# Kernel tuning notes

Hardware: AMD Instinct MI355X
Metric: run time of the kernel (lower is better)

## Reference

```python
import jax, jax.numpy as jnp
import numpy as np

B, T, C, H = 4, 2048, 1024, 16
D = C // H  # head_dim = 64


def setup_inputs() -> dict:
    key = jax.random.key(0)
    k1, k2, k3, k4 = jax.random.split(key, 4)
    x = jax.random.normal(k1, (B, T, C), dtype=jnp.float32)
    # realistic padding: each sequence has length in [T//2, T]
    lengths = jax.random.randint(k4, (B,), T // 2, T + 1)
    padding_mask = jnp.arange(T)[None, :] < lengths[:, None]  # True = keep
    # weights stored [in, out] (equivalent to torch Linear weight transposed)
    w_qkv = jax.random.normal(k2, (C, 3 * C), dtype=jnp.float32) * (C ** -0.5)
    w_out = jax.random.normal(k3, (C, C), dtype=jnp.float32) * (C ** -0.5)
    b_out = jnp.zeros((C,), dtype=jnp.float32)
    return {"x": x, "padding_mask": padding_mask, "w_qkv": w_qkv, "w_out": w_out, "b_out": b_out}


def reference(x, padding_mask, w_qkv, w_out, b_out):
    scale = D ** -0.5
    qkv = x @ w_qkv  # [B,T,3C]
    q, k, v = jnp.split(qkv, 3, axis=-1)

    def split_heads(t):
        return t.reshape(B, T, H, D).transpose(0, 2, 1, 3)  # [B,H,T,D]

    q, k, v = split_heads(q), split_heads(k), split_heads(v)
    attn = jnp.einsum("bhqd,bhkd->bhqk", q, k) * scale  # [B,H,T,T]
    mask = padding_mask[:, None, None, :]  # [B,1,1,T]
    attn = jnp.where(mask, attn, jnp.finfo(attn.dtype).min)
    attn = jax.nn.softmax(attn, axis=-1)
    # dropout is identity in eval mode
    out = jnp.einsum("bhqk,bhkd->bhqd", attn, v)  # [B,H,T,D]
    out = out.transpose(0, 2, 1, 3).reshape(B, T, C)
    return out @ w_out + b_out
```

## Files before the change

### kernel.cpp

```cpp
#include <hip/hip_runtime.h>
#include <hip/hip_bf16.h>

#define Bb 4
#define Tt 2048
#define Cc 1024
#define Hh 16

typedef unsigned short u16;
typedef __attribute__((ext_vector_type(8))) __bf16 bf16x8;
typedef __attribute__((ext_vector_type(4))) float  f32x4;

__device__ __forceinline__ u16 f2bf(float f) {
    union { float f; unsigned u; } v; v.f = f;
    unsigned r = v.u + 0x7fff + ((v.u >> 16) & 1);
    return (u16)(r >> 16);
}

__device__ __forceinline__ u16 f2bf_hw(float f) {
    __bf16 h = (__bf16)f;
    return *(u16*)&h;
}

__device__ __forceinline__ float fexp2(float x) {
#if __has_builtin(__builtin_amdgcn_exp2f)
    return __builtin_amdgcn_exp2f(x);
#else
    return __expf(x * 0.6931471805599453f);
#endif
}

__device__ __forceinline__ void gld_lds16(const void* g, void* l) {
    __builtin_amdgcn_global_load_lds(
        (__attribute__((address_space(1))) void*)(g),
        (__attribute__((address_space(3))) void*)(l),
        16, 0, 0);
}

__device__ __forceinline__ f32x4 mfma16(bf16x8 a, bf16x8 b, f32x4 c) {
    return __builtin_amdgcn_mfma_f32_16x16x32_bf16(a, b, c, 0, 0, 0);
}

__global__ void cast_f32_bf16(const float* __restrict__ in, u16* __restrict__ out, int n4) {
    int i = blockIdx.x * 256 + threadIdx.x;
    if (i < n4) {
        float4 v = ((const float4*)in)[i];
        uint2 o;
        o.x = (unsigned)f2bf_hw(v.x) | ((unsigned)f2bf_hw(v.y) << 16);
        o.y = (unsigned)f2bf_hw(v.z) | ((unsigned)f2bf_hw(v.w) << 16);
        ((uint2*)out)[i] = o;
    }
}

__global__ void castT_f32_bf16(const float* __restrict__ in, u16* __restrict__ out,
                               int K, int N) {
    __shared__ float Ls[64][65];
    const int n0 = blockIdx.x * 64, k0 = blockIdx.y * 64;
    const int t = threadIdx.x;
    #pragma unroll
    for (int s = 0; s < 4; ++s) {
        int idx = t + 256 * s;
        int r   = idx >> 4;
        int c4  = (idx & 15) * 4;
        float4 v = *(const float4*)&in[(size_t)(k0 + r) * N + n0 + c4];
        Ls[r][c4 + 0] = v.x; Ls[r][c4 + 1] = v.y;
        Ls[r][c4 + 2] = v.z; Ls[r][c4 + 3] = v.w;
    }
    __syncthreads();
    #pragma unroll
    for (int s = 0; s < 2; ++s) {
        int idx = t + 256 * s;
        int n   = idx >> 3;
        int kc  = (idx & 7) * 8;
        alignas(16) u16 tmp[8];
        #pragma unroll
        for (int i = 0; i < 8; ++i) tmp[i] = f2bf_hw(Ls[kc + i][n]);
        *(uint4*)&out[(size_t)(n0 + n) * K + k0 + kc] = *(const uint4*)tmp;
    }
}

__global__ void repack_vT(const u16* __restrict__ qkv, u16* __restrict__ vT) {
    const int t = threadIdx.x, w = t >> 6, lane = t & 63;
    const int tile = blockIdx.x, bh = blockIdx.y, b = bh >> 4, h = bh & 15;
    #pragma unroll
    for (int u = 0; u < 2; ++u) {
        int tc = tile * 64 + (2 * w + u) * 8;
        alignas(16) u16 tmp[8];
        #pragma unroll
        for (int i = 0; i < 8; ++i)
            tmp[i] = qkv[(size_t)(b * Tt + tc + i) * (3 * Cc) + 2 * Cc + h * 64 + lane];
        *(uint4*)&vT[((size_t)(bh * 64) + lane) * Tt + tc] = *(const uint4*)tmp;
    }
}

__global__ __launch_bounds__(256, 3) void gemm_bt_bf16(
    const u16* __restrict__ A, const u16* __restrict__ Bt,
    const float* __restrict__ bias,
    u16* __restrict__ outB, float* __restrict__ outF,
    int M, int N, int K)
{
    __shared__ u16 As[128 * 32];
    __shared__ u16 Bs[128 * 32];
    const int t = threadIdx.x;
    const int w = t >> 6, lane = t & 63;
    const int quad = lane >> 4, l16 = lane & 15;
    const int wr = w >> 1, wc = w & 1;
    const int m0 = blockIdx.y * 128, n0 = blockIdx.x * 128;

    int aoff[4], boff[4];
    #pragma unroll
    for (int i = 0; i < 4; ++i) {
        int rA = 64 * wr + 16 * i + l16;
        aoff[i] = rA * 32 + ((quad ^ ((rA >> 1) & 3)) * 8);
        int rB = 64 * wc + 16 * i + l16;
        boff[i] = rB * 32 + ((quad ^ ((rB >> 1) & 3)) * 8);
    }

    f32x4 acc[4][4] = {};

    for (int k0 = 0; k0 < K; k0 += 32) {
        __syncthreads();
        #pragma unroll
        for (int u = 0; u < 2; ++u) {
            const int i   = 2 * w + u;
            const int row = 16 * i + (lane >> 2);
            const int c   = (lane & 3) ^ ((row >> 1) & 3);
            gld_lds16(A  + (size_t)(m0 + row) * K + k0 + c * 8, (void*)(As + i * 512 + lane * 8));
            gld_lds16(Bt + (size_t)(n0 + row) * K + k0 + c * 8, (void*)(Bs + i * 512 + lane * 8));
        }
        asm volatile("s_waitcnt vmcnt(0)" ::: "memory");
        __syncthreads();

        bf16x8 af[4], bfr[4];
        #pragma unroll
        for (int i = 0; i < 4; ++i) af[i]  = *(const bf16x8*)&As[aoff[i]];
        #pragma unroll
        for (int j = 0; j < 4; ++j) bfr[j] = *(const bf16x8*)&Bs[boff[j]];
        #pragma unroll
        for (int i = 0; i < 4; ++i)
            #pragma unroll
            for (int j = 0; j < 4; ++j)
                acc[i][j] = mfma16(af[i], bfr[j], acc[i][j]);
    }

    const int rbase = m0 + 64 * wr + quad * 4;
    const int cbase = n0 + 64 * wc + l16;
    if (outF) {
        float bv[4];
        #pragma unroll
        for (int j = 0; j < 4; ++j) bv[j] = bias[cbase + 16 * j];
        #pragma unroll
        for (int i = 0; i < 4; ++i)
            #pragma unroll
            for (int r = 0; r < 4; ++r) {
                size_t ro = (size_t)(rbase + 16 * i + r) * N;
                #pragma unroll
                for (int j = 0; j < 4; ++j)
                    outF[ro + cbase + 16 * j] = acc[i][j][r] + bv[j];
            }
    } else {
        #pragma unroll
        for (int i = 0; i < 4; ++i)
            #pragma unroll
            for (int r = 0; r < 4; ++r) {
                size_t ro = (size_t)(rbase + 16 * i + r) * N;
                #pragma unroll
                for (int j = 0; j < 4; ++j)
                    outB[ro + cbase + 16 * j] = f2bf_hw(acc[i][j][r]);
            }
    }
}

__global__ __launch_bounds__(256, 3) void attn_mfma(
    const u16* __restrict__ qkv, const u16* __restrict__ vT,
    const int* __restrict__ mask, u16* __restrict__ outO)
{
    __shared__ u16 Qs[64 * 64];
    __shared__ u16 Ks[2][64 * 64];
    __shared__ u16 Vs[2][64 * 64];
    __shared__ u16 Ps[64 * 72];
    __shared__ int Lsh;

    const int t = threadIdx.x, w = t >> 6, lane = t & 63;
    const int quad = lane >> 4, l16 = lane & 15;
    const int qt = blockIdx.x, bh = blockIdx.y, b = bh >> 4, h = bh & 15;

    if (t == 0) Lsh = 0;
    __syncthreads();
    int partial = 0;
    #pragma unroll
    for (int k = 0; k < Tt / 256; ++k) partial += mask[b * Tt + t + 256 * k];
    #pragma unroll
    for (int off = 32; off > 0; off >>= 1) partial += __shfl_down(partial, off);
    if (lane == 0) atomicAdd(&Lsh, partial);

    const size_t kbase = (size_t)(b * Tt) * (3 * Cc) + Cc + h * 64;
    const size_t vbase = (size_t)(bh * 64) * Tt;

    const int srow = (lane >> 3);
    const int scol = (lane & 7);

    auto stage = [&](int ch, int buf) {
        const int kc = ch * 64;
        #pragma unroll
        for (int u = 0; u < 2; ++u) {
            const int i = 2 * w + u;
            const int row = 8 * i + srow;
            const int c = scol ^ (row & 7);
            gld_lds16(qkv + kbase + (size_t)(kc + row) * (3 * Cc) + c * 8,
                      (void*)(Ks[buf] + i * 512 + lane * 8));
            gld_lds16(vT + vbase + (size_t)row * Tt + kc + c * 8,
                      (void*)(Vs[buf] + i * 512 + lane * 8));
        }
    };

    const size_t qbase = (size_t)(b * Tt + qt * 64) * (3 * Cc) + h * 64;
    #pragma unroll
    for (int u = 0; u < 2; ++u) {
        const int i = 2 * w + u;
        const int row = 8 * i + srow;
        const int c = scol ^ (row & 7);
        gld_lds16(qkv + qbase + (size_t)row * (3 * Cc) + c * 8, (void*)(Qs + i * 512 + lane * 8));
    }
    stage(0, 0);
    asm volatile("s_waitcnt vmcnt(0)" ::: "memory");
    __syncthreads();
    const int L = Lsh;

    bf16x8 qf[2];
    {
        const int rq = 16 * w + l16;
        #pragma unroll
        for (int ks = 0; ks < 2; ++ks) {
            int c = quad + 4 * ks;
            qf[ks] = *(const bf16x8*)&Qs[rq * 64 + ((c ^ (rq & 7)) * 8)];
        }
    }
    int koff[4][2];
    #pragma unroll
    for (int i = 0; i < 4; ++i) {
        int r = 16 * i + l16;
        #pragma unroll
        for (int ks = 0; ks < 2; ++ks) {
            int c = quad + 4 * ks;
            koff[i][ks] = r * 64 + ((c ^ (r & 7)) * 8);
        }
    }
    const int poff0 = (16 * w + l16) * 72 + quad * 8;
    const int pw0   = (16 * w + quad * 4) * 72 + l16;

    f32x4 oacc[4] = {};
    float lsum[4] = {};
    const float c2 = 0.18033688011112042f;

    const int nfull = L >> 6;
    const int nch   = (L + 63) >> 6;

    for (int ch = 0; ch < nch; ++ch) {
        if (ch + 1 < nch) stage(ch + 1, (ch + 1) & 1);
        const u16* ks_ = Ks[ch & 1];
        const u16* vs_ = Vs[ch & 1];

        f32x4 s[4];
        #pragma unroll
        for (int jt = 0; jt < 4; ++jt) {
            f32x4 z = {0.f, 0.f, 0.f, 0.f};
            #pragma unroll
            for (int ks = 0; ks < 2; ++ks)
                z = mfma16(qf[ks], *(const bf16x8*)&ks_[koff[jt][ks]], z);
            s[jt] = z;
        }

        if (ch < nfull) {
            #pragma unroll
            for (int jt = 0; jt < 4; ++jt)
                #pragma unroll
                for (int r = 0; r < 4; ++r) {
                    float e = fexp2(s[jt][r] * c2);
                    lsum[r] += e;
                    Ps[pw0 + r * 72 + 16 * jt] = f2bf_hw(e);
                }
        } else {
            const int kc = ch * 64;
            #pragma unroll
            for (int jt = 0; jt < 4; ++jt) {
                const bool ok = (kc + 16 * jt + l16) < L;
                #pragma unroll
                for (int r = 0; r < 4; ++r) {
                    float e = ok ? fexp2(s[jt][r] * c2) : 0.f;
                    lsum[r] += e;
                    Ps[pw0 + r * 72 + 16 * jt] = f2bf_hw(e);
                }
            }
        }

        #pragma unroll
        for (int ks = 0; ks < 2; ++ks) {
            bf16x8 pf = *(const bf16x8*)&Ps[poff0 + 32 * ks];
            #pragma unroll
            for (int dt = 0; dt < 4; ++dt)
                oacc[dt] = mfma16(pf, *(const bf16x8*)&vs_[koff[dt][ks]], oacc[dt]);
        }

        asm volatile("s_waitcnt vmcnt(0)" ::: "memory");
        __syncthreads();
    }

    #pragma unroll
    for (int r = 0; r < 4; ++r) {
        float v = lsum[r];
        v += __shfl_xor(v, 1); v += __shfl_xor(v, 2);
        v += __shfl_xor(v, 4); v += __shfl_xor(v, 8);
        lsum[r] = v;
    }

    const int tok0 = qt * 64 + 16 * w + quad * 4;
    #pragma unroll
    for (int r = 0; r < 4; ++r) {
        const float inv = 1.f / lsum[r];
        const size_t ro = (size_t)(b * Tt + tok0 + r) * Cc + h * 64;
        #pragma unroll
        for (int dt = 0; dt < 4; ++dt)
            outO[ro + 16 * dt + l16] = f2bf_hw(oacc[dt][r] * inv);
    }
}

extern "C" void kernel_launch(void* const* d_in, const int* in_sizes, int n_in,
                              void* d_out, int out_size, void* d_ws, size_t ws_size,
                              hipStream_t stream) {
    const float* x     = (const float*)d_in[0];
    const int*   mask  = (const int*)  d_in[1];
    const float* w_qkv = (const float*)d_in[2];
    const float* w_out = (const float*)d_in[3];
    const float* b_out = (const float*)d_in[4];
    float*       outp  = (float*)d_out;

    const int M = Bb * Tt;
    char* ws = (char*)d_ws;
    u16* xb     = (u16*)(ws);
    u16* wqkvT  = (u16*)(ws + (16u << 20));
    u16* woutT  = (u16*)(ws + (22u << 20));
    u16* qkv    = (u16*)(ws + (24u << 20));
    u16* vT     = (u16*)(ws + (72u << 20));
    u16* attnO  = (u16*)(ws + (88u << 20));

    cast_f32_bf16<<<(M * Cc / 4 + 255) / 256, 256, 0, stream>>>(x, xb, M * Cc / 4);
    castT_f32_bf16<<<dim3(3 * Cc / 64, Cc / 64), 256, 0, stream>>>(w_qkv, wqkvT, Cc, 3 * Cc);
    castT_f32_bf16<<<dim3(Cc / 64, Cc / 64), 256, 0, stream>>>(w_out, woutT, Cc, Cc);

    gemm_bt_bf16<<<dim3(3 * Cc / 128, M / 128), 256, 0, stream>>>(
        xb, wqkvT, nullptr, qkv, nullptr, M, 3 * Cc, Cc);

    repack_vT<<<dim3(Tt / 64, Bb * Hh), 256, 0, stream>>>(qkv, vT);

    attn_mfma<<<dim3(Tt / 64, Bb * Hh), 256, 0, stream>>>(qkv, vT, mask, attnO);

    gemm_bt_bf16<<<dim3(Cc / 128, M / 128), 256, 0, stream>>>(
        attnO, woutT, b_out, nullptr, outp, M, Cc, Cc);
}
```

Measured before the change: 295.4 us.

## Double attention query tile to 128 rows per block and transpose score MFMA

Each attention block now handles 128 query rows instead of 64, with every wave owning two 16-row query sub-tiles. Each staged K/V chunk is therefore reused across twice as many queries, halving K/V global and LDS traffic per query. K and V fragments are loaded into registers once per chunk and shared by both sub-tiles. The score MFMA operands are swapped so each lane writes four consecutive probabilities as one packed 8-byte LDS store. The costs are higher register pressure (occupancy hint drops from 3 to 2) and half as many blocks in the grid.

```diff
diff --git a/kernel.cpp b/kernel.cpp
--- a/kernel.cpp
+++ b/kernel.cpp
@@ -9,12 +9,6 @@
 typedef unsigned short u16;
 typedef __attribute__((ext_vector_type(8))) __bf16 bf16x8;
 typedef __attribute__((ext_vector_type(4))) float  f32x4;
-
-__device__ __forceinline__ u16 f2bf(float f) {
-    union { float f; unsigned u; } v; v.f = f;
-    unsigned r = v.u + 0x7fff + ((v.u >> 16) & 1);
-    return (u16)(r >> 16);
-}
 
 __device__ __forceinline__ u16 f2bf_hw(float f) {
     __bf16 h = (__bf16)f;
@@ -170,14 +164,14 @@
     }
 }
 
-__global__ __launch_bounds__(256, 3) void attn_mfma(
+__global__ __launch_bounds__(256, 2) void attn_mfma(
     const u16* __restrict__ qkv, const u16* __restrict__ vT,
     const int* __restrict__ mask, u16* __restrict__ outO)
 {
-    __shared__ u16 Qs[64 * 64];
+    __shared__ u16 Qs[128 * 64];
     __shared__ u16 Ks[2][64 * 64];
     __shared__ u16 Vs[2][64 * 64];
-    __shared__ u16 Ps[64 * 72];
+    __shared__ u16 Ps[128 * 72];
     __shared__ int Lsh;
 
     const int t = threadIdx.x, w = t >> 6, lane = t & 63;
@@ -195,9 +189,7 @@
 
     const size_t kbase = (size_t)(b * Tt) * (3 * Cc) + Cc + h * 64;
     const size_t vbase = (size_t)(bh * 64) * Tt;
-
-    const int srow = (lane >> 3);
-    const int scol = (lane & 7);
+    const int srow = lane >> 3, scol = lane & 7;
 
     auto stage = [&](int ch, int buf) {
         const int kc = ch * 64;
@@ -213,10 +205,10 @@
         }
     };
 
-    const size_t qbase = (size_t)(b * Tt + qt * 64) * (3 * Cc) + h * 64;
-    #pragma unroll
-    for (int u = 0; u < 2; ++u) {
-        const int i = 2 * w + u;
+    const size_t qbase = (size_t)(b * Tt + qt * 128) * (3 * Cc) + h * 64;
+    #pragma unroll
+    for (int u = 0; u < 4; ++u) {
+        const int i = 4 * w + u;
         const int row = 8 * i + srow;
         const int c = scol ^ (row & 7);
         gld_lds16(qkv + qbase + (size_t)row * (3 * Cc) + c * 8, (void*)(Qs + i * 512 + lane * 8));
@@ -226,30 +218,26 @@
     __syncthreads();
     const int L = Lsh;
 
-    bf16x8 qf[2];
-    {
-        const int rq = 16 * w + l16;
-        #pragma unroll
-        for (int ks = 0; ks < 2; ++ks) {
-            int c = quad + 4 * ks;
-            qf[ks] = *(const bf16x8*)&Qs[rq * 64 + ((c ^ (rq & 7)) * 8)];
-        }
+    bf16x8 qf[2][2];
+    #pragma unroll
+    for (int qq = 0; qq < 2; ++qq) {
+        const int rq = 32 * w + 16 * qq + l16;
+        #pragma unroll
+        for (int ks = 0; ks < 2; ++ks)
+            qf[qq][ks] = *(const bf16x8*)&Qs[rq * 64 + (((quad + 4 * ks) ^ (rq & 7)) * 8)];
     }
     int koff[4][2];
     #pragma unroll
     for (int i = 0; i < 4; ++i) {
         int r = 16 * i + l16;
         #pragma unroll
-        for (int ks = 0; ks < 2; ++ks) {
-            int c = quad + 4 * ks;
-            koff[i][ks] = r * 64 + ((c ^ (r & 7)) * 8);
-        }
-    }
-    const int poff0 = (16 * w + l16) * 72 + quad * 8;
-    const int pw0   = (16 * w + quad * 4) * 72 + l16;
-
-    f32x4 oacc[4] = {};
-    float lsum[4] = {};
+        for (int ks = 0; ks < 2; ++ks)
+            koff[i][ks] = r * 64 + (((quad + 4 * ks) ^ (r & 7)) * 8);
+    }
+    const int prow = 32 * w + l16;
+
+    f32x4 oacc[2][4] = {};
+    float lsum[2] = {};
     const float c2 = 0.18033688011112042f;
 
     const int nfull = L >> 6;
@@ -260,68 +248,89 @@
         const u16* ks_ = Ks[ch & 1];
         const u16* vs_ = Vs[ch & 1];
 
-        f32x4 s[4];
-        #pragma unroll
-        for (int jt = 0; jt < 4; ++jt) {
-            f32x4 z = {0.f, 0.f, 0.f, 0.f};
-            #pragma unroll
-            for (int ks = 0; ks < 2; ++ks)
-                z = mfma16(qf[ks], *(const bf16x8*)&ks_[koff[jt][ks]], z);
-            s[jt] = z;
+        bf16x8 kf[4][2], vf[4][2];
+        #pragma unroll
+        for (int i = 0; i < 4; ++i)
+            #pragma unroll
+            for (int ks = 0; ks < 2; ++ks) {
+                kf[i][ks] = *(const bf16x8*)&ks_[koff[i][ks]];
+                vf[i][ks] = *(const bf16x8*)&vs_[koff[i][ks]];
+            }
+
+        #pragma unroll
+        for (int qq = 0; qq < 2; ++qq) {
+            f32x4 st[4];
+            #pragma unroll
+            for (int jt = 0; jt < 4; ++jt) {
+                f32x4 z = {0.f, 0.f, 0.f, 0.f};
+                z = mfma16(kf[jt][0], qf[qq][0], z);
+                st[jt] = mfma16(kf[jt][1], qf[qq][1], z);
+            }
+            if (ch < nfull) {
+                #pragma unroll
+                for (int jt = 0; jt < 4; ++jt) {
+                    float e0 = fexp2(st[jt][0] * c2);
+                    float e1 = fexp2(st[jt][1] * c2);
+                    float e2 = fexp2(st[jt][2] * c2);
+                    float e3 = fexp2(st[jt][3] * c2);
+                    lsum[qq] += (e0 + e1) + (e2 + e3);
+                    uint2 pk;
+                    pk.x = (unsigned)f2bf_hw(e0) | ((unsigned)f2bf_hw(e1) << 16);
+                    pk.y = (unsigned)f2bf_hw(e2) | ((unsigned)f2bf_hw(e3) << 16);
+                    *(uint2*)&Ps[(prow + 16 * qq) * 72 + 16 * jt + quad * 4] = pk;
+                }
+            } else {
+                const int kc = ch * 64;
+                #pragma unroll
+                for (int jt = 0; jt < 4; ++jt) {
+                    const int kb = kc + 16 * jt + quad * 4;
+                    float e[4];
+                    #pragma unroll
+                    for (int r = 0; r < 4; ++r) {
+                        e[r] = (kb + r < L) ? fexp2(st[jt][r] * c2) : 0.f;
+                        lsum[qq] += e[r];
+                    }
+                    uint2 pk;
+                    pk.x = (unsigned)f2bf_hw(e[0]) | ((unsigned)f2bf_hw(e[1]) << 16);
+                    pk.y = (unsigned)f2bf_hw(e[2]) | ((unsigned)f2bf_hw(e[3]) << 16);
+                    *(uint2*)&Ps[(prow + 16 * qq) * 72 + 16 * jt + quad * 4] = pk;
+                }
+            }
         }
 
-        if (ch < nfull) {
-            #pragma unroll
-            for (int jt = 0; jt < 4; ++jt)
-                #pragma unroll
-                for (int r = 0; r < 4; ++r) {
-                    float e = fexp2(s[jt][r] * c2);
-                    lsum[r] += e;
-                    Ps[pw0 + r * 72 + 16 * jt] = f2bf_hw(e);
-                }
-        } else {
-            const int kc = ch * 64;
-            #pragma unroll
-            for (int jt = 0; jt < 4; ++jt) {
-                const bool ok = (kc + 16 * jt + l16) < L;
-                #pragma unroll
-                for (int r = 0; r < 4; ++r) {
-                    float e = ok ? fexp2(s[jt][r] * c2) : 0.f;
-                    lsum[r] += e;
-                    Ps[pw0 + r * 72 + 16 * jt] = f2bf_hw(e);
-                }
-            }
-        }
-
-        #pragma unroll
-        for (int ks = 0; ks < 2; ++ks) {
-            bf16x8 pf = *(const bf16x8*)&Ps[poff0 + 32 * ks];
-            #pragma unroll
-            for (int dt = 0; dt < 4; ++dt)
-                oacc[dt] = mfma16(pf, *(const bf16x8*)&vs_[koff[dt][ks]], oacc[dt]);
-        }
+        #pragma unroll
+        for (int qq = 0; qq < 2; ++qq)
+            #pragma unroll
+            for (int ks = 0; ks < 2; ++ks) {
+                bf16x8 pf = *(const bf16x8*)&Ps[(prow + 16 * qq) * 72 + quad * 8 + 32 * ks];
+                #pragma unroll
+                for (int dt = 0; dt < 4; ++dt)
+                    oacc[qq][dt] = mfma16(pf, vf[dt][ks], oacc[qq][dt]);
+            }
 
         asm volatile("s_waitcnt vmcnt(0)" ::: "memory");
         __syncthreads();
     }
 
     #pragma unroll
-    for (int r = 0; r < 4; ++r) {
-        float v = lsum[r];
-        v += __shfl_xor(v, 1); v += __shfl_xor(v, 2);
-        v += __shfl_xor(v, 4); v += __shfl_xor(v, 8);
-        lsum[r] = v;
-    }
-
-    const int tok0 = qt * 64 + 16 * w + quad * 4;
-    #pragma unroll
-    for (int r = 0; r < 4; ++r) {
-        const float inv = 1.f / lsum[r];
-        const size_t ro = (size_t)(b * Tt + tok0 + r) * Cc + h * 64;
-        #pragma unroll
-        for (int dt = 0; dt < 4; ++dt)
-            outO[ro + 16 * dt + l16] = f2bf_hw(oacc[dt][r] * inv);
-    }
+    for (int qq = 0; qq < 2; ++qq) {
+        float v = lsum[qq];
+        v += __shfl_xor(v, 16);
+        v += __shfl_xor(v, 32);
+        lsum[qq] = v;
+    }
+
+    const int orow0 = qt * 128 + 32 * w;
+    #pragma unroll
+    for (int qq = 0; qq < 2; ++qq)
+        #pragma unroll
+        for (int r = 0; r < 4; ++r) {
+            const float inv = 1.f / __shfl(lsum[qq], quad * 4 + r);
+            const size_t ro = (size_t)(b * Tt + orow0 + 16 * qq + quad * 4 + r) * Cc + h * 64;
+            #pragma unroll
+            for (int dt = 0; dt < 4; ++dt)
+                outO[ro + 16 * dt + l16] = f2bf_hw(oacc[qq][dt][r] * inv);
+        }
 }
 
 extern "C" void kernel_launch(void* const* d_in, const int* in_sizes, int n_in,
@@ -352,7 +361,7 @@
 
     repack_vT<<<dim3(Tt / 64, Bb * Hh), 256, 0, stream>>>(qkv, vT);
 
-    attn_mfma<<<dim3(Tt / 64, Bb * Hh), 256, 0, stream>>>(qkv, vT, mask, attnO);
+    attn_mfma<<<dim3(Tt / 128, Bb * Hh), 256, 0, stream>>>(qkv, vT, mask, attnO);
 
     gemm_bt_bf16<<<dim3(Cc / 128, M / 128), 256, 0, stream>>>(
         attnO, woutT, b_out, nullptr, outp, M, Cc, Cc);
```

Result: faster. 279.0 us (-5.6%).
